# Kernel optimization log

Hardware: AMD Instinct MI355X
Metric: run time of the kernel (lower is better)

The kernel has to match this reference:

```python
import jax, jax.numpy as jnp
import numpy as np

B, S, DIM, H = 4, 2048, 1024, 16
DEPTH = DIM // H


def setup_inputs() -> dict:
    key = jax.random.key(0)
    ks = jax.random.split(key, 12)
    s = 0.02
    return {
        "Q": jax.random.normal(ks[0], (B, S, DIM), jnp.float32),
        "K": jax.random.normal(ks[1], (B, S, DIM), jnp.float32),
        "V": jax.random.normal(ks[2], (B, S, DIM), jnp.float32),
        "mask": jax.random.randint(ks[3], (B, 1, 1, S), 0, 2).astype(jnp.float32),
        "Wq": jax.random.normal(ks[4], (DIM, DIM), jnp.float32) * s,
        "bq": jnp.zeros((DIM,), jnp.float32),
        "Wk": jax.random.normal(ks[5], (DIM, DIM), jnp.float32) * s,
        "bk": jnp.zeros((DIM,), jnp.float32),
        "Wv": jax.random.normal(ks[6], (DIM, DIM), jnp.float32) * s,
        "bv": jnp.zeros((DIM,), jnp.float32),
        "Wo": jax.random.normal(ks[7], (DIM, DIM), jnp.float32) * s,
        "bo": jnp.zeros((DIM,), jnp.float32),
    }


def _split_heads(x):
    # [B,S,DIM] -> [B,H,S,DEPTH]
    return x.reshape(x.shape[0], x.shape[1], H, DEPTH).transpose(0, 2, 1, 3)


def reference(Q, K, V, mask, Wq, bq, Wk, bk, Wv, bv, Wo, bo):
    q = _split_heads(Q @ Wq + bq)
    k = _split_heads(K @ Wk + bk)
    v = _split_heads(V @ Wv + bv)
    # scaled dot-product attention; note original scales by sqrt(depth) = last dim of K after split
    logits = jnp.einsum("bhqd,bhkd->bhqk", q, k) / jnp.sqrt(jnp.float32(DEPTH))
    logits = logits + mask * -1e9
    attn = jax.nn.softmax(logits, axis=-1)
    ctx = jnp.einsum("bhqk,bhkd->bhqd", attn, v)
    ctx = ctx.transpose(0, 2, 1, 3).reshape(Q.shape[0], Q.shape[1], DIM)
    return ctx @ Wo + bo
```

## Files before the change

kernel.cpp:

```cpp
#include <hip/hip_runtime.h>

typedef short s16x8 __attribute__((ext_vector_type(8)));
typedef short s16x4 __attribute__((ext_vector_type(4)));
typedef float f32x4 __attribute__((ext_vector_type(4)));

#define MFMA32(a, b, c) __builtin_amdgcn_mfma_f32_16x16x32_bf16((a), (b), (c), 0, 0, 0)

__device__ __forceinline__ void stage16(const unsigned short* g, unsigned short* l) {
#if defined(__HIP_DEVICE_COMPILE__)
  __builtin_amdgcn_global_load_lds((const __attribute__((address_space(1))) unsigned int*)g,
                                   (__attribute__((address_space(3))) unsigned int*)l, 16, 0, 0);
#endif
}

__device__ __forceinline__ unsigned short f2b(float f) {
  unsigned int u = __builtin_bit_cast(unsigned int, f);
  unsigned int r = u + 0x7FFFu + ((u >> 16) & 1u);
  return (unsigned short)(r >> 16);
}
__device__ __forceinline__ unsigned int pk2(float a, float b) {
#if defined(__HIP_DEVICE_COMPILE__)
  unsigned int ua = __builtin_bit_cast(unsigned int, a);
  unsigned int ub = __builtin_bit_cast(unsigned int, b);
  ua += 0x7FFFu + ((ua >> 16) & 1u);
  ub += 0x7FFFu + ((ub >> 16) & 1u);
  return __builtin_amdgcn_perm(ub, ua, 0x07060302u);
#else
  return (unsigned int)f2b(a) | ((unsigned int)f2b(b) << 16);
#endif
}
__device__ __forceinline__ float fast_exp2(float x) {
#if defined(__HIP_DEVICE_COMPILE__) && __has_builtin(__builtin_amdgcn_exp2f)
  return __builtin_amdgcn_exp2f(x);
#else
  return exp2f(x);
#endif
}

__global__ __launch_bounds__(256) void castq(const float* __restrict__ X,
                                             unsigned short* __restrict__ Y) {
  int i = blockIdx.x * 256 + threadIdx.x;
  float4 f0 = ((const float4*)X)[i * 2];
  float4 f1 = ((const float4*)X)[i * 2 + 1];
  uint4 u;
  u.x = pk2(f0.x, f0.y);
  u.y = pk2(f0.z, f0.w);
  u.z = pk2(f1.x, f1.y);
  u.w = pk2(f1.z, f1.w);
  ((uint4*)Y)[i] = u;
}

__global__ void wtrans(const float* __restrict__ W0, const float* __restrict__ W1,
                       const float* __restrict__ W2, const float* __restrict__ W3,
                       unsigned short* __restrict__ T0, unsigned short* __restrict__ T1,
                       unsigned short* __restrict__ T2, unsigned short* __restrict__ T3) {
  const float* W;
  unsigned short* T;
  switch (blockIdx.z) {
    case 0: W = W0; T = T0; break;
    case 1: W = W1; T = T1; break;
    case 2: W = W2; T = T2; break;
    default: W = W3; T = T3; break;
  }
  __shared__ float tile[32][33];
  const int n0 = blockIdx.x << 5;
  const int k0 = blockIdx.y << 5;
  const int tx = threadIdx.x;
  const int ty = threadIdx.y;
#pragma unroll
  for (int j = 0; j < 4; ++j)
    tile[ty + 8 * j][tx] = W[(size_t)(k0 + ty + 8 * j) * 1024 + n0 + tx];
  __syncthreads();
#pragma unroll
  for (int j = 0; j < 4; ++j)
    T[(size_t)(n0 + ty + 8 * j) * 1024 + k0 + tx] = f2b(tile[tx][ty + 8 * j]);
}

template <int MODE>
__global__ __launch_bounds__(256, 2) void gemm_bt(const unsigned short* __restrict__ A,
                                                  const unsigned short* __restrict__ Bt,
                                                  const float* __restrict__ bias,
                                                  void* __restrict__ Cout, float oscale) {
  __shared__ __align__(16) unsigned short As[128 * 32];
  __shared__ __align__(16) unsigned short Bs[128 * 32];
  const int n0 = blockIdx.x * 128;
  const int m0 = blockIdx.y * 128;
  const int tid = threadIdx.x;
  const int w = tid >> 6;
  const int lane = tid & 63;
  const int lr = lane & 15;
  const int lg = lane >> 4;
  const int wm = (w >> 1) << 6;
  const int wn = (w & 1) << 6;

  const int srow = w * 16 + (lane >> 2);
  const int sseg = lane & 3;
  const unsigned short* Ag0 = A + (size_t)(m0 + srow) * 1024 + sseg * 8;
  const unsigned short* Ag1 = A + (size_t)(m0 + 64 + srow) * 1024 + sseg * 8;
  const unsigned short* Bg0 = Bt + (size_t)(n0 + srow) * 1024 + sseg * 8;
  const unsigned short* Bg1 = Bt + (size_t)(n0 + 64 + srow) * 1024 + sseg * 8;
  unsigned short* Al0 = &As[(w * 16) * 32];
  unsigned short* Al1 = &As[(64 + w * 16) * 32];
  unsigned short* Bl0 = &Bs[(w * 16) * 32];
  unsigned short* Bl1 = &Bs[(64 + w * 16) * 32];

  f32x4 acc[4][4];
#pragma unroll
  for (int i = 0; i < 4; ++i)
#pragma unroll
    for (int j = 0; j < 4; ++j) {
      f32x4 z = {0.f, 0.f, 0.f, 0.f};
      acc[i][j] = z;
    }

  for (int k0 = 0; k0 < 1024; k0 += 32) {
    stage16(Ag0 + k0, Al0);
    stage16(Ag1 + k0, Al1);
    stage16(Bg0 + k0, Bl0);
    stage16(Bg1 + k0, Bl1);
    __syncthreads();
    s16x8 af[4], bfr[4];
#pragma unroll
    for (int mt = 0; mt < 4; ++mt) af[mt] = *(const s16x8*)&As[(wm + mt * 16 + lr) * 32 + lg * 8];
#pragma unroll
    for (int nt = 0; nt < 4; ++nt) bfr[nt] = *(const s16x8*)&Bs[(wn + nt * 16 + lr) * 32 + lg * 8];
#pragma unroll
    for (int mt = 0; mt < 4; ++mt)
#pragma unroll
      for (int nt = 0; nt < 4; ++nt)
        acc[mt][nt] = MFMA32(af[mt], bfr[nt], acc[mt][nt]);
    __syncthreads();
  }

  float bcol[4];
#pragma unroll
  for (int nt = 0; nt < 4; ++nt) bcol[nt] = bias[n0 + wn + nt * 16 + lr];

#pragma unroll
  for (int mt = 0; mt < 4; ++mt)
#pragma unroll
    for (int nt = 0; nt < 4; ++nt)
#pragma unroll
      for (int r = 0; r < 4; ++r) {
        float v = (acc[mt][nt][r] + bcol[nt]) * oscale;
        int row = m0 + wm + mt * 16 + lg * 4 + r;
        int col = n0 + wn + nt * 16 + lr;
        if constexpr (MODE == 0) {
          int b = row >> 11, s = row & 2047, hh = col >> 6, d = col & 63;
          ((unsigned short*)Cout)[(((size_t)(b * 16 + hh) * 2048 + s) << 6) + d] = f2b(v);
        } else if constexpr (MODE == 1) {
          int b = row >> 11, s = row & 2047, hh = col >> 6, d = col & 63;
          ((unsigned short*)Cout)[(((size_t)(b * 16 + hh) * 64 + d) << 11) + s] = f2b(v);
        } else {
          ((float*)Cout)[(size_t)row * 1024 + col] = v;
        }
      }
}

__global__ __launch_bounds__(256, 4) void flash_attn(const unsigned short* __restrict__ qh,
                                                     const unsigned short* __restrict__ kh,
                                                     const unsigned short* __restrict__ vt,
                                                     const float* __restrict__ mask,
                                                     unsigned short* __restrict__ ctx) {
  const float c2 = 1.4426950408889634e9f;
  const int id = blockIdx.x;
  const int bh = id & 63;
  const int qtile = id >> 6;
  const int b = bh >> 4;
  const int h = bh & 15;
  const int q0 = qtile << 7;
  const int tid = threadIdx.x;
  const int w = tid >> 6;
  const int lane = tid & 63;
  const int lr = lane & 15;
  const int lg = lane >> 4;

  __shared__ __align__(16) unsigned short Ks[2 * 64 * 64];
  __shared__ __align__(16) unsigned short Vs[2 * 64 * 64];

  const unsigned short* qbase = qh + ((size_t)bh * 2048 + q0 + w * 32) * 64;
  const unsigned short* kbase = kh + (size_t)bh * 2048 * 64;
  const unsigned short* vbase = vt + (size_t)bh * 64 * 2048;
  const float* mbase = mask + b * 2048;

  const int rowc = lane >> 3;
  const int gseg = (lane & 7) ^ rowc;
  const unsigned short* kg0 = kbase + (size_t)(w * 16 + rowc) * 64 + gseg * 8;
  const unsigned short* kg1 = kbase + (size_t)(w * 16 + 8 + rowc) * 64 + gseg * 8;
  const unsigned short* vg0 = vbase + (size_t)(w * 16 + rowc) * 2048 + gseg * 8;
  const unsigned short* vg1 = vbase + (size_t)(w * 16 + 8 + rowc) * 2048 + gseg * 8;
  unsigned short* kl0 = &Ks[(w * 16 + 0) * 64];
  unsigned short* kl1 = &Ks[(w * 16 + 8) * 64];
  unsigned short* vl0 = &Vs[(w * 16 + 0) * 64];
  unsigned short* vl1 = &Vs[(w * 16 + 8) * 64];

  s16x8 qf[2][2];
#pragma unroll
  for (int qt = 0; qt < 2; ++qt)
#pragma unroll
    for (int kk = 0; kk < 2; ++kk)
      qf[qt][kk] = *(const s16x8*)(qbase + (qt * 16 + lr) * 64 + kk * 32 + lg * 8);

  const s16x8 ones8 = {(short)0x3F80, (short)0x3F80, (short)0x3F80, (short)0x3F80,
                       (short)0x3F80, (short)0x3F80, (short)0x3F80, (short)0x3F80};

  f32x4 o_acc[2][4];
  f32x4 l_acc[2];
#pragma unroll
  for (int qt = 0; qt < 2; ++qt) {
    f32x4 z = {0.f, 0.f, 0.f, 0.f};
    l_acc[qt] = z;
#pragma unroll
    for (int dt = 0; dt < 4; ++dt) o_acc[qt][dt] = z;
  }

  stage16(kg0, kl0);
  stage16(kg1, kl1);
  stage16(vg0, vl0);
  stage16(vg1, vl1);
  asm volatile("s_waitcnt vmcnt(0)\n\ts_barrier" ::: "memory");

  int cur = 0;
  for (int t0 = 0; t0 < 2048; t0 += 64) {
    if (t0 + 64 < 2048) {
      const int nb = (cur ^ 1) * 4096;
      stage16(kg0 + (size_t)(t0 + 64) * 64, kl0 + nb);
      stage16(kg1 + (size_t)(t0 + 64) * 64, kl1 + nb);
      stage16(vg0 + (t0 + 64), vl0 + nb);
      stage16(vg1 + (t0 + 64), vl1 + nb);
    }
    float4 mk[4];
#pragma unroll
    for (int kt = 0; kt < 4; ++kt) mk[kt] = *(const float4*)(mbase + t0 + kt * 16 + lg * 4);

    const int cb = cur * 4096;
    const int sw = lr & 7;
    unsigned int pw[4][2][2];
#pragma unroll
    for (int kt = 0; kt < 4; ++kt) {
      const int krow = kt * 16 + lr;
      s16x8 kf0 = *(const s16x8*)&Ks[cb + krow * 64 + ((lg ^ sw) * 8)];
      s16x8 kf1 = *(const s16x8*)&Ks[cb + krow * 64 + (((4 + lg) ^ sw) * 8)];
      float ml0 = mk[kt].x * c2, ml1 = mk[kt].y * c2;
      float ml2 = mk[kt].z * c2, ml3 = mk[kt].w * c2;
#pragma unroll
      for (int qt = 0; qt < 2; ++qt) {
        f32x4 s = {0.f, 0.f, 0.f, 0.f};
        s = MFMA32(kf0, qf[qt][0], s);
        s = MFMA32(kf1, qf[qt][1], s);
        pw[kt][qt][0] = pk2(fast_exp2(s[0] - ml0), fast_exp2(s[1] - ml1));
        pw[kt][qt][1] = pk2(fast_exp2(s[2] - ml2), fast_exp2(s[3] - ml3));
      }
    }

#pragma unroll
    for (int c = 0; c < 2; ++c) {
      s16x8 pb[2];
#pragma unroll
      for (int qt = 0; qt < 2; ++qt) {
        uint4 u;
        u.x = pw[2 * c][qt][0];
        u.y = pw[2 * c][qt][1];
        u.z = pw[2 * c + 1][qt][0];
        u.w = pw[2 * c + 1][qt][1];
        pb[qt] = __builtin_bit_cast(s16x8, u);
        l_acc[qt] = MFMA32(ones8, pb[qt], l_acc[qt]);
      }
      const int plo = ((c << 2) | (lg >> 1)) ^ sw;
      const int phi = ((c << 2) | 2 | (lg >> 1)) ^ sw;
      const int sub = (lg & 1) * 4;
#pragma unroll
      for (int dt = 0; dt < 4; ++dt) {
        const int d = dt * 16 + lr;
        s16x4 vlo = *(const s16x4*)&Vs[cb + d * 64 + plo * 8 + sub];
        s16x4 vhi = *(const s16x4*)&Vs[cb + d * 64 + phi * 8 + sub];
        s16x8 vf = __builtin_shufflevector(vlo, vhi, 0, 1, 2, 3, 4, 5, 6, 7);
#pragma unroll
        for (int qt = 0; qt < 2; ++qt) o_acc[qt][dt] = MFMA32(vf, pb[qt], o_acc[qt][dt]);
      }
    }

    asm volatile("s_waitcnt vmcnt(0)\n\ts_barrier" ::: "memory");
    cur ^= 1;
  }

#pragma unroll
  for (int qt = 0; qt < 2; ++qt) {
    float inv = 1.0f / l_acc[qt][0];
    int q = q0 + w * 32 + qt * 16 + lr;
    unsigned short* cp = ctx + ((size_t)(b * 2048 + q) * 16 + h) * 64 + lg * 4;
#pragma unroll
    for (int dt = 0; dt < 4; ++dt) {
      f32x4 o = o_acc[qt][dt];
      uint2 u;
      u.x = pk2(o[0] * inv, o[1] * inv);
      u.y = pk2(o[2] * inv, o[3] * inv);
      *(uint2*)(cp + dt * 16) = u;
    }
  }
}

extern "C" void kernel_launch(void* const* d_in, const int* in_sizes, int n_in,
                              void* d_out, int out_size, void* d_ws, size_t ws_size,
                              hipStream_t stream) {
  (void)in_sizes; (void)n_in; (void)out_size; (void)ws_size;
  const float* Q = (const float*)d_in[0];
  const float* K = (const float*)d_in[1];
  const float* V = (const float*)d_in[2];
  const float* mask = (const float*)d_in[3];
  const float* Wq = (const float*)d_in[4];
  const float* bq = (const float*)d_in[5];
  const float* Wk = (const float*)d_in[6];
  const float* bk = (const float*)d_in[7];
  const float* Wv = (const float*)d_in[8];
  const float* bv = (const float*)d_in[9];
  const float* Wo = (const float*)d_in[10];
  const float* bo = (const float*)d_in[11];

  char* ws = (char*)d_ws;
  unsigned short* wqt = (unsigned short*)(ws + (size_t)0);
  unsigned short* wkt = (unsigned short*)(ws + ((size_t)2 << 20));
  unsigned short* wvt = (unsigned short*)(ws + ((size_t)4 << 20));
  unsigned short* wot = (unsigned short*)(ws + ((size_t)6 << 20));
  unsigned short* qhb = (unsigned short*)(ws + ((size_t)8 << 20));
  unsigned short* khb = (unsigned short*)(ws + ((size_t)24 << 20));
  unsigned short* vtb = (unsigned short*)(ws + ((size_t)40 << 20));
  unsigned short* tmp = (unsigned short*)(ws + ((size_t)56 << 20));
  unsigned short* ctx = tmp;

  wtrans<<<dim3(32, 32, 4), dim3(32, 8), 0, stream>>>(Wq, Wk, Wv, Wo, wqt, wkt, wvt, wot);

  const float qscale = 0.18033688011112042f;
  dim3 gg(8, 64), bb(256);
  const int castBlocks = (8192 * 1024) / (256 * 8);

  castq<<<castBlocks, 256, 0, stream>>>(Q, tmp);
  gemm_bt<0><<<gg, bb, 0, stream>>>(tmp, wqt, bq, qhb, qscale);
  castq<<<castBlocks, 256, 0, stream>>>(K, tmp);
  gemm_bt<0><<<gg, bb, 0, stream>>>(tmp, wkt, bk, khb, 1.0f);
  castq<<<castBlocks, 256, 0, stream>>>(V, tmp);
  gemm_bt<1><<<gg, bb, 0, stream>>>(tmp, wvt, bv, vtb, 1.0f);

  flash_attn<<<dim3(1024), dim3(256), 0, stream>>>(qhb, khb, vtb, mask, ctx);

  gemm_bt<2><<<gg, bb, 0, stream>>>(ctx, wot, bo, d_out, 1.0f);
}
```

Before: 381.3 us.

## Double-buffer LDS staging in projection GEMM to overlap loads with MFMA

The projection GEMM now keeps two LDS buffers for the A and B tiles. While MFMAs run on the current K-slice, it issues direct global-to-LDS loads for the next slice, using one waitcnt plus barrier per iteration instead of two syncthreads. Launch bounds are raised to 3 blocks per CU to allow more occupancy despite doubled shared memory. The risk is register pressure from the tighter bound and a missing lgkmcnt wait before the barrier, which could let the next prefetch overwrite a buffer still being read.

New measurement: 389.3 us. 2.1% more time.

```diff
diff --git a/kernel.cpp b/kernel.cpp
--- a/kernel.cpp
+++ b/kernel.cpp
@@ -77,12 +77,12 @@
 }
 
 template <int MODE>
-__global__ __launch_bounds__(256, 2) void gemm_bt(const unsigned short* __restrict__ A,
+__global__ __launch_bounds__(256, 3) void gemm_bt(const unsigned short* __restrict__ A,
                                                   const unsigned short* __restrict__ Bt,
                                                   const float* __restrict__ bias,
                                                   void* __restrict__ Cout, float oscale) {
-  __shared__ __align__(16) unsigned short As[128 * 32];
-  __shared__ __align__(16) unsigned short Bs[128 * 32];
+  __shared__ __align__(16) unsigned short As[2 * 128 * 32];
+  __shared__ __align__(16) unsigned short Bs[2 * 128 * 32];
   const int n0 = blockIdx.x * 128;
   const int m0 = blockIdx.y * 128;
   const int tid = threadIdx.x;
@@ -113,23 +113,36 @@
       acc[i][j] = z;
     }
 
+  stage16(Ag0, Al0);
+  stage16(Ag1, Al1);
+  stage16(Bg0, Bl0);
+  stage16(Bg1, Bl1);
+  asm volatile("s_waitcnt vmcnt(0)\n\ts_barrier" ::: "memory");
+
+  int cur = 0;
   for (int k0 = 0; k0 < 1024; k0 += 32) {
-    stage16(Ag0 + k0, Al0);
-    stage16(Ag1 + k0, Al1);
-    stage16(Bg0 + k0, Bl0);
-    stage16(Bg1 + k0, Bl1);
-    __syncthreads();
+    if (k0 + 32 < 1024) {
+      const int nb = (cur ^ 1) * 4096;
+      stage16(Ag0 + k0 + 32, Al0 + nb);
+      stage16(Ag1 + k0 + 32, Al1 + nb);
+      stage16(Bg0 + k0 + 32, Bl0 + nb);
+      stage16(Bg1 + k0 + 32, Bl1 + nb);
+    }
+    const int cb = cur * 4096;
     s16x8 af[4], bfr[4];
 #pragma unroll
-    for (int mt = 0; mt < 4; ++mt) af[mt] = *(const s16x8*)&As[(wm + mt * 16 + lr) * 32 + lg * 8];
-#pragma unroll
-    for (int nt = 0; nt < 4; ++nt) bfr[nt] = *(const s16x8*)&Bs[(wn + nt * 16 + lr) * 32 + lg * 8];
+    for (int mt = 0; mt < 4; ++mt)
+      af[mt] = *(const s16x8*)&As[cb + (wm + mt * 16 + lr) * 32 + lg * 8];
+#pragma unroll
+    for (int nt = 0; nt < 4; ++nt)
+      bfr[nt] = *(const s16x8*)&Bs[cb + (wn + nt * 16 + lr) * 32 + lg * 8];
 #pragma unroll
     for (int mt = 0; mt < 4; ++mt)
 #pragma unroll
       for (int nt = 0; nt < 4; ++nt)
         acc[mt][nt] = MFMA32(af[mt], bfr[nt], acc[mt][nt]);
-    __syncthreads();
+    asm volatile("s_waitcnt vmcnt(0)\n\ts_barrier" ::: "memory");
+    cur ^= 1;
   }
 
   float bcol[4];
```
